# Optimization experiments

Hardware: AMD Instinct MI355X
Metric: run time of the kernel (lower is better)

Reference implementation:

```python
import jax, jax.numpy as jnp
import numpy as np

N_NODES = 100000
N_EDGES = 1600000
C = 64       # in_channels == filters
K = 3        # Chebyshev order
EPS = 1e-5   # InstanceNorm eps


def setup_inputs() -> dict:
    key = jax.random.key(0)
    ks = jax.random.split(key, 8)
    x = jax.random.normal(ks[0], (N_NODES, C), dtype=jnp.float32)
    edge_index = jax.random.randint(ks[1], (2, N_EDGES), 0, N_NODES, dtype=jnp.int64)
    scale = 1.0 / np.sqrt(C)
    W1 = jax.random.normal(ks[2], (K, C, C), dtype=jnp.float32) * scale
    b1 = jnp.zeros((C,), dtype=jnp.float32)
    W2 = jax.random.normal(ks[3], (K, C, C), dtype=jnp.float32) * scale
    b2 = jnp.zeros((C,), dtype=jnp.float32)
    return {"x": x, "edge_index": edge_index, "W1": W1, "b1": b1, "W2": W2, "b2": b2}


def _cheb_conv(x, src, dst, w_edge, W, b, n):
    # PyG ChebConv, norm='sym', lambda_max=2: L_hat = -D^{-1/2} A D^{-1/2}
    def prop(h):  # h: [N, C] -> L_hat @ h via gather -> weight -> scatter-add
        return jax.ops.segment_sum(w_edge[:, None] * h[src], dst, num_segments=n)
    Tx0 = x
    Tx1 = prop(x)
    Tx2 = 2.0 * prop(Tx1) - Tx0
    return Tx0 @ W[0] + Tx1 @ W[1] + Tx2 @ W[2] + b


def _instance_norm(h):
    # PyG InstanceNorm (single graph, affine=False): normalize over nodes per channel
    m = h.mean(axis=0, keepdims=True)
    v = h.var(axis=0, keepdims=True)
    return (h - m) * jax.lax.rsqrt(v + EPS)


def reference(x, edge_index, W1, b1, W2, b2):
    n = x.shape[0]
    src, dst = edge_index[0], edge_index[1]
    ones = jnp.ones((src.shape[0],), dtype=x.dtype)
    deg = jax.ops.segment_sum(ones, dst, num_segments=n)
    safe = jnp.where(deg > 0, deg, 1.0)
    dinv = jnp.where(deg > 0, jax.lax.rsqrt(safe), 0.0)
    w_edge = -dinv[src] * dinv[dst]  # scaled-Laplacian edge weights
    h = _instance_norm(jax.nn.relu(_cheb_conv(x, src, dst, w_edge, W1, b1, n)))
    h = _instance_norm(jax.nn.relu(_cheb_conv(h, src, dst, w_edge, W2, b2, n)))
    return h
```

## Files before the change

kernel.cpp:

```cpp
#include <hip/hip_runtime.h>
#include <hip/hip_fp16.h>

#define NCH 64
#define EPS 1e-5f
#define SBANKS 32
#define BSHIFT 8
#define NHIST 256
#define BINCAP 6400
#define PADRES 2048
#define RSHIFT 14
#define SRCMASK 0x1FFFFu
#define QW_SCALE 32767.0f
#define QW_INV (1.0f/32767.0f)

typedef _Float16 f16x8 __attribute__((ext_vector_type(8)));
typedef float f32x4 __attribute__((ext_vector_type(4)));

__global__ __launch_bounds__(256) void k_front(const float* __restrict__ x, __half* __restrict__ xh,
                                               int castTotal, int castB,
                                               const float* __restrict__ W1, _Float16* __restrict__ Wb1,
                                               const float* __restrict__ W2, _Float16* __restrict__ Wb2,
                                               const int* __restrict__ dst, int* __restrict__ cnt,
                                               int E, int per, int nbuck) {
    int bid = blockIdx.x;
    if (bid < castB) {
        int i = (bid * 256 + threadIdx.x) * 4;
        if (i < castTotal) {
            float4 f = *(const float4*)(x + i);
            __half2* o = (__half2*)(xh + i);
            o[0] = __floats2half2_rn(f.x, f.y);
            o[1] = __floats2half2_rn(f.z, f.w);
        }
        return;
    }
    if (bid < castB + 96) {
        int wb = bid - castB;
        const float* W = (wb < 48) ? W1 : W2;
        _Float16* Wb = (wb < 48) ? Wb1 : Wb2;
        int idx = (wb % 48) * 256 + threadIdx.x;
        int j = idx & 7;
        int lane = (idx >> 3) & 63;
        int tk = idx >> 9;
        int tile = tk / 6, kk = tk % 6;
        int k = kk * 32 + (lane >> 4) * 8 + j;
        int n = tile * 16 + (lane & 15);
        Wb[idx] = (_Float16)W[k * 64 + n];
        return;
    }
    __shared__ int lh[512];
    int hb = bid - castB - 96;
    for (int t = threadIdx.x; t < nbuck; t += 256) lh[t] = 0;
    __syncthreads();
    int lo = hb * per, hi = min(E, lo + per);
    for (int e = lo + threadIdx.x; e < hi; e += 256)
        atomicAdd(&lh[dst[e] >> BSHIFT], 1);
    __syncthreads();
    for (int t = threadIdx.x; t < nbuck; t += 256)
        if (lh[t]) atomicAdd(&cnt[t], lh[t]);
}

__global__ void k_bscan(const int* __restrict__ cnt, int* __restrict__ gbase,
                        int* __restrict__ gcur, int nbuck, int E) {
    __shared__ int s[512];
    int t = threadIdx.x;
    int v = (t < nbuck) ? cnt[t] : 0;
    s[t] = v;
    __syncthreads();
    for (int off = 1; off < 512; off <<= 1) {
        int add = (t >= off) ? s[t - off] : 0;
        __syncthreads();
        s[t] += add;
        __syncthreads();
    }
    if (t < nbuck) { int ex = s[t] - v; gbase[t] = ex; gcur[t] = ex; }
    if (t == 0) gbase[nbuck] = E;
}

__global__ __launch_bounds__(256) void k_bin(const int* __restrict__ src,
                                             const int* __restrict__ dst,
                                             int* __restrict__ gcur,
                                             int2* __restrict__ binned, int E, int per, int nbuck) {
    __shared__ int lh[512];
    __shared__ int lsc[512];
    __shared__ int lbase[512];
    __shared__ int lcur[512];
    __shared__ int2 sedge[BINCAP];
    int t = threadIdx.x;
    for (int i = t; i < 512; i += 256) lh[i] = 0;
    __syncthreads();
    int lo = blockIdx.x * per, hi = min(E, lo + per);
    for (int e = lo + t; e < hi; e += 256)
        atomicAdd(&lh[dst[e] >> BSHIFT], 1);
    __syncthreads();
    int v0 = lh[t], v1 = lh[t + 256];
    lsc[t] = v0; lsc[t + 256] = v1;
    __syncthreads();
    for (int off = 1; off < 512; off <<= 1) {
        int a0 = (t >= off) ? lsc[t - off] : 0;
        int a1 = (t + 256 >= off) ? lsc[t + 256 - off] : 0;
        __syncthreads();
        lsc[t] += a0; lsc[t + 256] += a1;
        __syncthreads();
    }
    lsc[t] -= v0; lsc[t + 256] -= v1;
    if (t < nbuck && v0) lbase[t] = atomicAdd(&gcur[t], v0);
    if (t + 256 < nbuck && v1) lbase[t + 256] = atomicAdd(&gcur[t + 256], v1);
    lcur[t] = lsc[t]; lcur[t + 256] = lsc[t + 256];
    __syncthreads();
    for (int e = lo + t; e < hi; e += 256) {
        int d = dst[e];
        int b = d >> BSHIFT;
        int pos = atomicAdd(&lcur[b], 1);
        sedge[pos] = make_int2(src[e], d);
    }
    __syncthreads();
    int cntE = hi - lo;
    for (int i = t; i < cntE; i += 256) {
        int2 sd = sedge[i];
        int b = sd.y >> BSHIFT;
        binned[lbase[b] + (i - lsc[b])] = sd;
    }
}

__global__ __launch_bounds__(256) void k_bucket(const int2* __restrict__ binned,
                                                const int* __restrict__ gbase,
                                                float* __restrict__ dinv,
                                                int2* __restrict__ rowinfo,
                                                unsigned int* __restrict__ csr, int N, int nbuck) {
    __shared__ int hist8[256 * 8];
    __shared__ int cur8[256 * 8];
    __shared__ int ldeg[256];
    __shared__ int ltmp[256];
    int b = blockIdx.x;
    int t = threadIdx.x;
    int nodeLo = b << BSHIFT;
    int nHere = min(256, N - nodeLo);
    int e0 = gbase[b], e1 = gbase[b + 1];
    int pb = (gbase[b] + b * PADRES + 7) & ~7;
    for (int i = t; i < 256 * 8; i += 256) hist8[i] = 0;
    __syncthreads();
    for (int e = e0 + t; e < e1; e += 256) {
        int2 sd = binned[e];
        atomicAdd(&hist8[((sd.y - nodeLo) << 3) + (sd.x >> RSHIFT)], 1);
    }
    __syncthreads();
    int c[8], deg = 0;
#pragma unroll
    for (int r = 0; r < 8; r++) { c[r] = hist8[(t << 3) + r]; deg += c[r]; }
    int pdeg = (deg + 7) & ~7;
    ldeg[t] = deg;
    if (t < nHere) dinv[nodeLo + t] = (deg > 0) ? rsqrtf((float)deg) : 0.0f;
    ltmp[t] = pdeg;
    __syncthreads();
    for (int off = 1; off < 256; off <<= 1) {
        int add = (t >= off) ? ltmp[t - off] : 0;
        __syncthreads();
        ltmp[t] += add;
        __syncthreads();
    }
    int lstart = ltmp[t] - pdeg;
    if (t < nHere) rowinfo[nodeLo + t] = make_int2(pb + lstart, pdeg);
    int run = lstart;
#pragma unroll
    for (int r = 0; r < 8; r++) { cur8[(t << 3) + r] = run; run += c[r]; }
    __syncthreads();
    for (int e = e0 + t; e < e1; e += 256) {
        int2 sd = binned[e];
        int dl = sd.y - nodeLo;
        int pos = atomicAdd(&cur8[(dl << 3) + (sd.x >> RSHIFT)], 1);
        unsigned int dd = (unsigned int)min(ldeg[dl], 32767);
        csr[pb + pos] = (unsigned int)sd.x | (dd << 17);
    }
    __syncthreads();
    if (t < nHere) {
        int d = ldeg[t];
        int pd = (d + 7) & ~7;
        if (pd > d) {
            unsigned int fill = (d > 0) ? (csr[pb + lstart] & SRCMASK) : 0u;
            for (int i = d; i < pd; i++) csr[pb + lstart + i] = fill;
        }
    }
}

__global__ void k_weights(unsigned int* __restrict__ csr, const float* __restrict__ dinv, int PE) {
    int e = blockIdx.x * blockDim.x + threadIdx.x;
    if (e < PE) {
        unsigned int v = csr[e];
        unsigned int d = v >> 17;
        if (d == 0) return;
        unsigned int s = v & SRCMASK;
        float aw = dinv[s] * rsqrtf((float)d);
        unsigned int qw = (unsigned int)(aw * QW_SCALE + 0.5f);
        csr[e] = s | (qw << 17);
    }
}


#define GATH(A0,A1,A2,A3,A4,A5,A6,A7, C0, C1) \
    A0 = *(const uint4*)(hb + (size_t)(C0.x & SRCMASK) * NCH); \
    A1 = *(const uint4*)(hb + (size_t)(C0.y & SRCMASK) * NCH); \
    A2 = *(const uint4*)(hb + (size_t)(C0.z & SRCMASK) * NCH); \
    A3 = *(const uint4*)(hb + (size_t)(C0.w & SRCMASK) * NCH); \
    A4 = *(const uint4*)(hb + (size_t)(C1.x & SRCMASK) * NCH); \
    A5 = *(const uint4*)(hb + (size_t)(C1.y & SRCMASK) * NCH); \
    A6 = *(const uint4*)(hb + (size_t)(C1.z & SRCMASK) * NCH); \
    A7 = *(const uint4*)(hb + (size_t)(C1.w & SRCMASK) * NCH);

#define FMA1(A, W) { \
    float2 f; \
    f = __half22float2(*(const __half2*)&A.x); acc[0] = fmaf(W, f.x, acc[0]); acc[1] = fmaf(W, f.y, acc[1]); \
    f = __half22float2(*(const __half2*)&A.y); acc[2] = fmaf(W, f.x, acc[2]); acc[3] = fmaf(W, f.y, acc[3]); \
    f = __half22float2(*(const __half2*)&A.z); acc[4] = fmaf(W, f.x, acc[4]); acc[5] = fmaf(W, f.y, acc[5]); \
    f = __half22float2(*(const __half2*)&A.w); acc[6] = fmaf(W, f.x, acc[6]); acc[7] = fmaf(W, f.y, acc[7]); }

#define FMA8(A0,A1,A2,A3,A4,A5,A6,A7, C0, C1) { \
    float w0 = -(float)(C0.x >> 17) * QW_INV; \
    float w1 = -(float)(C0.y >> 17) * QW_INV; \
    float w2 = -(float)(C0.z >> 17) * QW_INV; \
    float w3 = -(float)(C0.w >> 17) * QW_INV; \
    float w4 = -(float)(C1.x >> 17) * QW_INV; \
    float w5 = -(float)(C1.y >> 17) * QW_INV; \
    float w6 = -(float)(C1.z >> 17) * QW_INV; \
    float w7 = -(float)(C1.w >> 17) * QW_INV; \
    sw += ((w0 + w1) + (w2 + w3)) + ((w4 + w5) + (w6 + w7)); \
    FMA1(A0, w0) FMA1(A1, w1) FMA1(A2, w2) FMA1(A3, w3) \
    FMA1(A4, w4) FMA1(A5, w5) FMA1(A6, w6) FMA1(A7, w7) }

__global__ __launch_bounds__(256) void k_prop(const __half* __restrict__ h,
                                              const int2* __restrict__ rowinfo,
                                              const unsigned int* __restrict__ csr,
                                              const __half* __restrict__ tx0,
                                              __half* __restrict__ y, int N,
                                              const float* __restrict__ gstats,
                                              const float* __restrict__ tstats) {
    int lane = threadIdx.x & 63;
    int wv = (blockIdx.x * 256 + threadIdx.x) >> 6;
    int g = lane >> 3, li = lane & 7;
    int node = wv * 8 + g;
    int e = 0, eN = 0;
    if (node < N) {
        int2 info = rowinfo[node];
        e = info.x;
        eN = info.x + info.y;
    }
    float acc[8] = {0.f, 0.f, 0.f, 0.f, 0.f, 0.f, 0.f, 0.f};
    float sw = 0.0f;
    const __half* hb = h + li * 8;
    uint4 c0, c1, d0, d1;
    uint4 a0, a1, a2, a3, a4, a5, a6, a7;
    uint4 b0, b1, b2, b3, b4, b5, b6, b7;
    if (e < eN) {
        c0 = *(const uint4*)(csr + e);
        c1 = *(const uint4*)(csr + e + 4);
        int en = (e + 8 < eN) ? e + 8 : e;
        d0 = *(const uint4*)(csr + en);
        d1 = *(const uint4*)(csr + en + 4);
        GATH(a0, a1, a2, a3, a4, a5, a6, a7, c0, c1);
    }
    while (e + 8 < eN) {
        GATH(b0, b1, b2, b3, b4, b5, b6, b7, d0, d1);
        bool hasT = (e + 16 < eN);
        int enT = hasT ? e + 16 : e;
        uint4 t0 = *(const uint4*)(csr + enT);
        uint4 t1 = *(const uint4*)(csr + enT + 4);
        FMA8(a0, a1, a2, a3, a4, a5, a6, a7, c0, c1);
        if (hasT) { GATH(a0, a1, a2, a3, a4, a5, a6, a7, t0, t1); }
        int enD = (e + 24 < eN) ? e + 24 : e;
        uint4 u0 = *(const uint4*)(csr + enD);
        uint4 u1 = *(const uint4*)(csr + enD + 4);
        FMA8(b0, b1, b2, b3, b4, b5, b6, b7, d0, d1);
        c0 = t0; c1 = t1; d0 = u0; d1 = u1;
        e += 16;
    }
    if (e < eN) { FMA8(a0, a1, a2, a3, a4, a5, a6, a7, c0, c1); }
    if (node >= N) return;
    if (gstats != nullptr) {
        float4 m0 = *(const float4*)(gstats + li * 8);
        float4 m1 = *(const float4*)(gstats + li * 8 + 4);
        float4 r0 = *(const float4*)(gstats + 64 + li * 8);
        float4 r1 = *(const float4*)(gstats + 64 + li * 8 + 4);
        acc[0] = r0.x * (acc[0] - m0.x * sw);
        acc[1] = r0.y * (acc[1] - m0.y * sw);
        acc[2] = r0.z * (acc[2] - m0.z * sw);
        acc[3] = r0.w * (acc[3] - m0.w * sw);
        acc[4] = r1.x * (acc[4] - m1.x * sw);
        acc[5] = r1.y * (acc[5] - m1.y * sw);
        acc[6] = r1.z * (acc[6] - m1.z * sw);
        acc[7] = r1.w * (acc[7] - m1.w * sw);
    }
    if (tx0 != nullptr) {
        uint4 tq = *(const uint4*)(tx0 + (size_t)node * NCH + li * 8);
        float tv[8];
        float2 f;
        f = __half22float2(*(__half2*)&tq.x); tv[0] = f.x; tv[1] = f.y;
        f = __half22float2(*(__half2*)&tq.y); tv[2] = f.x; tv[3] = f.y;
        f = __half22float2(*(__half2*)&tq.z); tv[4] = f.x; tv[5] = f.y;
        f = __half22float2(*(__half2*)&tq.w); tv[6] = f.x; tv[7] = f.y;
        if (tstats != nullptr) {
            float4 m0 = *(const float4*)(tstats + li * 8);
            float4 m1 = *(const float4*)(tstats + li * 8 + 4);
            float4 r0 = *(const float4*)(tstats + 64 + li * 8);
            float4 r1 = *(const float4*)(tstats + 64 + li * 8 + 4);
            tv[0] = (tv[0] - m0.x) * r0.x; tv[1] = (tv[1] - m0.y) * r0.y;
            tv[2] = (tv[2] - m0.z) * r0.z; tv[3] = (tv[3] - m0.w) * r0.w;
            tv[4] = (tv[4] - m1.x) * r1.x; tv[5] = (tv[5] - m1.y) * r1.y;
            tv[6] = (tv[6] - m1.z) * r1.z; tv[7] = (tv[7] - m1.w) * r1.w;
        }
#pragma unroll
        for (int j = 0; j < 8; j++) acc[j] = 2.0f * acc[j] - tv[j];
    }
    uint4 o;
    __half2 hh;
    hh = __floats2half2_rn(acc[0], acc[1]); o.x = *(unsigned int*)&hh;
    hh = __floats2half2_rn(acc[2], acc[3]); o.y = *(unsigned int*)&hh;
    hh = __floats2half2_rn(acc[4], acc[5]); o.z = *(unsigned int*)&hh;
    hh = __floats2half2_rn(acc[6], acc[7]); o.w = *(unsigned int*)&hh;
    *(uint4*)(y + (size_t)node * NCH + li * 8) = o;
}

template <typename TOUT>
__global__ __launch_bounds__(256) void k_dmm(const __half* __restrict__ tx0,
                                             const __half* __restrict__ tx1,
                                             const __half* __restrict__ tx2,
                                             const _Float16* __restrict__ Wb,
                                             const float* __restrict__ b,
                                             TOUT* __restrict__ out,
                                             float* __restrict__ statsP, int N,
                                             const float* __restrict__ tstats) {
    __shared__ float sred[64];
    __shared__ float sq[64];
    int t = threadIdx.x;
    int w = t >> 6;
    int lane = t & 63;
    if (t < 64) { sred[t] = 0.f; sq[t] = 0.f; }
    __syncthreads();

    int nb16 = blockIdx.x * 64 + w * 16;
    int m = lane & 15, q = lane >> 4;
    int row = nb16 + m;
    int rowC = (row < N) ? row : 0;
    const __half* base0 = tx0 + (size_t)rowC * NCH;
    const __half* base1 = tx1 + (size_t)rowC * NCH;
    const __half* base2 = tx2 + (size_t)rowC * NCH;

    f32x4 acc[4];
#pragma unroll
    for (int tile = 0; tile < 4; tile++) acc[tile] = (f32x4){0.f, 0.f, 0.f, 0.f};

#pragma unroll
    for (int kk = 0; kk < 6; kk++) {
        const __half* ap = (kk < 2 ? base0 : (kk < 4 ? base1 : base2)) + (kk & 1) * 32 + q * 8;
        f16x8 a = *(const f16x8*)ap;
        if (kk < 2 && tstats != nullptr) {
            int cbase = (kk & 1) * 32 + q * 8;
#pragma unroll
            for (int j = 0; j < 8; j++) {
                float v = (float)a[j];
                a[j] = (_Float16)((v - tstats[cbase + j]) * tstats[64 + cbase + j]);
            }
        }
#pragma unroll
        for (int tile = 0; tile < 4; tile++) {
            f16x8 bf = *(const f16x8*)(Wb + ((size_t)(tile * 6 + kk) * 64 + lane) * 8);
            acc[tile] = __builtin_amdgcn_mfma_f32_16x16x32_f16(a, bf, acc[tile], 0, 0, 0);
        }
    }

#pragma unroll
    for (int tile = 0; tile < 4; tile++) {
        int ch = tile * 16 + m;
        float bb = b[ch];
        float s = 0.f, qq = 0.f;
#pragma unroll
        for (int r = 0; r < 4; r++) {
            int node = nb16 + q * 4 + r;
            float v = fmaxf(acc[tile][r] + bb, 0.f);
            if (node < N) {
                out[(size_t)node * NCH + ch] = (TOUT)v;
                s += v;
                qq = fmaf(v, v, qq);
            }
        }
        s += __shfl_xor(s, 16, 64);  s += __shfl_xor(s, 32, 64);
        qq += __shfl_xor(qq, 16, 64); qq += __shfl_xor(qq, 32, 64);
        if (q == 0) { atomicAdd(&sred[ch], s); atomicAdd(&sq[ch], qq); }
    }
    __syncthreads();
    if (t < 64) {
        int bank = blockIdx.x & (SBANKS - 1);
        atomicAdd(&statsP[bank * 128 + t], sred[t]);
        atomicAdd(&statsP[bank * 128 + 64 + t], sq[t]);
    }
}

__global__ void k_final(float* __restrict__ statsP, float invN) {
    int c = threadIdx.x;
    float S = 0.f, Q = 0.f;
    for (int k = 0; k < SBANKS; k++) {
        S += statsP[k * 128 + c];
        Q += statsP[k * 128 + 64 + c];
    }
    float m = S * invN;
    float var = Q * invN - m * m;
    statsP[SBANKS * 128 + c] = m;
    statsP[SBANKS * 128 + 64 + c] = rsqrtf(var + EPS);
}

__global__ void k_norm_hf(const __half* __restrict__ a, float* __restrict__ o,
                          const float* __restrict__ statsP, int total) {
    int i = blockIdx.x * blockDim.x + threadIdx.x;
    if (i >= total) return;
    int lane = i & 63;
    o[i] = (__half2float(a[i]) - statsP[SBANKS * 128 + lane]) * statsP[SBANKS * 128 + 64 + lane];
}

extern "C" void kernel_launch(void* const* d_in, const int* in_sizes, int n_in,
                              void* d_out, int out_size, void* d_ws, size_t ws_size,
                              hipStream_t stream) {
    const float* x  = (const float*)d_in[0];
    const int*   ei = (const int*)d_in[1];
    const float* W1 = (const float*)d_in[2];
    const float* b1 = (const float*)d_in[3];
    const float* W2 = (const float*)d_in[4];
    const float* b2 = (const float*)d_in[5];
    float* out = (float*)d_out;

    const int N = in_sizes[0] / NCH;
    const int E = in_sizes[1] / 2;
    const int* src = ei;
    const int* dst = ei + E;
    const int nbuck = (N + 255) >> BSHIFT;
    const int PE = E + nbuck * PADRES + 8;

    char* p = (char*)d_ws;
    auto alloc = [&](size_t bytes) {
        void* r = (void*)p;
        p += ((bytes + 255) / 256) * 256;
        return r;
    };
    float*  dinv     = (float*)alloc((size_t)131072 * 4);
    int2*   rowinfo  = (int2*)alloc((size_t)N * 8);
    unsigned int* csr = (unsigned int*)alloc((size_t)PE * 4);
    __half* xh       = (__half*)alloc((size_t)N * NCH * 2);
    __half* Tx1      = (__half*)alloc((size_t)N * NCH * 2);
    __half* Tx2      = (__half*)alloc((size_t)N * NCH * 2);
    __half* A        = (__half*)alloc((size_t)N * NCH * 2);
    __half* A2       = (__half*)alloc((size_t)N * NCH * 2);
    _Float16* Wb1    = (_Float16*)alloc(12288 * 2);
    _Float16* Wb2    = (_Float16*)alloc(12288 * 2);
    int*    gbase    = (int*)alloc((size_t)(nbuck + 1) * 4);
    int*    gcur     = (int*)alloc((size_t)nbuck * 4);
    const int statsFloats = SBANKS * 128 + 128;
    int*    cnt      = (int*)alloc((size_t)nbuck * 4 + (size_t)2 * statsFloats * 4);
    float*  stats1   = (float*)(cnt + nbuck);
    float*  stats2   = stats1 + statsFloats;
    const float* nrm1 = stats1 + SBANKS * 128;

    int2* binned = (int2*)Tx1;

    hipMemsetAsync(cnt, 0, (size_t)nbuck * 4 + (size_t)2 * statsFloats * 4, stream);

    const int TB = 256;
    int nbin = (E + BINCAP - 1) / BINCAP;
    if (nbin < 256) nbin = 256;
    const int perBin = (E + nbin - 1) / nbin;
    const int perH = (E + NHIST - 1) / NHIST;
    const int castTotal = N * NCH;
    const int castB = (castTotal / 4 + TB - 1) / TB;
    k_front<<<castB + 96 + NHIST, TB, 0, stream>>>(x, xh, castTotal, castB,
                                                   W1, Wb1, W2, Wb2,
                                                   dst, cnt, E, perH, nbuck);
    k_bscan<<<1, 512, 0, stream>>>(cnt, gbase, gcur, nbuck, E);
    k_bin<<<nbin, TB, 0, stream>>>(src, dst, gcur, binned, E, perBin, nbuck);
    k_bucket<<<nbuck, TB, 0, stream>>>(binned, gbase, dinv, rowinfo, csr, N, nbuck);
    k_weights<<<(PE + TB - 1) / TB, TB, 0, stream>>>(csr, dinv, PE);

    const int propWaves = (N + 7) / 8;
    const int propBlocks = (propWaves + 3) / 4;
    const int dmmBlocks = (N + 63) / 64;
    const int normBlocks = (N * NCH + TB - 1) / TB;
    const float invN = 1.0f / (float)N;

    k_prop<<<propBlocks, TB, 0, stream>>>(xh, rowinfo, csr, nullptr, Tx1, N, nullptr, nullptr);
    k_prop<<<propBlocks, TB, 0, stream>>>(Tx1, rowinfo, csr, xh, Tx2, N, nullptr, nullptr);
    k_dmm<__half><<<dmmBlocks, TB, 0, stream>>>(xh, Tx1, Tx2, Wb1, b1, A, stats1, N, nullptr);
    k_final<<<1, 64, 0, stream>>>(stats1, invN);

    k_prop<<<propBlocks, TB, 0, stream>>>(A, rowinfo, csr, nullptr, Tx1, N, nrm1, nullptr);
    k_prop<<<propBlocks, TB, 0, stream>>>(Tx1, rowinfo, csr, A, Tx2, N, nullptr, nrm1);
    k_dmm<__half><<<dmmBlocks, TB, 0, stream>>>(A, Tx1, Tx2, Wb2, b2, A2, stats2, N, nrm1);
    k_final<<<1, 64, 0, stream>>>(stats2, invN);
    k_norm_hf<<<normBlocks, TB, 0, stream>>>(A2, out, stats2, N * NCH);
}
```

Measured before the change: 341.7 us.

## Simplify prop gather loop, vectorize final norm, halve bin capacity

Result: faster. 328.8 us (-3.8%).

```diff
diff --git a/kernel.cpp b/kernel.cpp
--- a/kernel.cpp
+++ b/kernel.cpp
@@ -6,7 +6,8 @@
 #define SBANKS 32
 #define BSHIFT 8
 #define NHIST 256
-#define BINCAP 6400
+#define BINCAP 3200
+#define NBINMIN 512
 #define PADRES 2048
 #define RSHIFT 14
 #define SRCMASK 0x1FFFFu
@@ -237,42 +238,22 @@
     int wv = (blockIdx.x * 256 + threadIdx.x) >> 6;
     int g = lane >> 3, li = lane & 7;
     int node = wv * 8 + g;
-    int e = 0, eN = 0;
+    int e = 0, e1 = 0;
     if (node < N) {
         int2 info = rowinfo[node];
         e = info.x;
-        eN = info.x + info.y;
+        e1 = info.x + info.y;
     }
     float acc[8] = {0.f, 0.f, 0.f, 0.f, 0.f, 0.f, 0.f, 0.f};
     float sw = 0.0f;
     const __half* hb = h + li * 8;
-    uint4 c0, c1, d0, d1;
-    uint4 a0, a1, a2, a3, a4, a5, a6, a7;
-    uint4 b0, b1, b2, b3, b4, b5, b6, b7;
-    if (e < eN) {
-        c0 = *(const uint4*)(csr + e);
-        c1 = *(const uint4*)(csr + e + 4);
-        int en = (e + 8 < eN) ? e + 8 : e;
-        d0 = *(const uint4*)(csr + en);
-        d1 = *(const uint4*)(csr + en + 4);
+    for (; e < e1; e += 8) {
+        uint4 c0 = *(const uint4*)(csr + e);
+        uint4 c1 = *(const uint4*)(csr + e + 4);
+        uint4 a0, a1, a2, a3, a4, a5, a6, a7;
         GATH(a0, a1, a2, a3, a4, a5, a6, a7, c0, c1);
-    }
-    while (e + 8 < eN) {
-        GATH(b0, b1, b2, b3, b4, b5, b6, b7, d0, d1);
-        bool hasT = (e + 16 < eN);
-        int enT = hasT ? e + 16 : e;
-        uint4 t0 = *(const uint4*)(csr + enT);
-        uint4 t1 = *(const uint4*)(csr + enT + 4);
         FMA8(a0, a1, a2, a3, a4, a5, a6, a7, c0, c1);
-        if (hasT) { GATH(a0, a1, a2, a3, a4, a5, a6, a7, t0, t1); }
-        int enD = (e + 24 < eN) ? e + 24 : e;
-        uint4 u0 = *(const uint4*)(csr + enD);
-        uint4 u1 = *(const uint4*)(csr + enD + 4);
-        FMA8(b0, b1, b2, b3, b4, b5, b6, b7, d0, d1);
-        c0 = t0; c1 = t1; d0 = u0; d1 = u1;
-        e += 16;
-    }
-    if (e < eN) { FMA8(a0, a1, a2, a3, a4, a5, a6, a7, c0, c1); }
+    }
     if (node >= N) return;
     if (gstats != nullptr) {
         float4 m0 = *(const float4*)(gstats + li * 8);
@@ -407,11 +388,24 @@
 }
 
 __global__ void k_norm_hf(const __half* __restrict__ a, float* __restrict__ o,
-                          const float* __restrict__ statsP, int total) {
+                          const float* __restrict__ statsP, int total8) {
     int i = blockIdx.x * blockDim.x + threadIdx.x;
-    if (i >= total) return;
-    int lane = i & 63;
-    o[i] = (__half2float(a[i]) - statsP[SBANKS * 128 + lane]) * statsP[SBANKS * 128 + 64 + lane];
+    if (i >= total8) return;
+    int c0 = (i & 7) * 8;
+    const float* mp = statsP + SBANKS * 128;
+    float4 m0 = *(const float4*)(mp + c0);
+    float4 m1 = *(const float4*)(mp + c0 + 4);
+    float4 r0 = *(const float4*)(mp + 64 + c0);
+    float4 r1 = *(const float4*)(mp + 64 + c0 + 4);
+    uint4 q = *(const uint4*)(a + (size_t)i * 8);
+    float2 f;
+    float4 o0, o1;
+    f = __half22float2(*(__half2*)&q.x); o0.x = (f.x - m0.x) * r0.x; o0.y = (f.y - m0.y) * r0.y;
+    f = __half22float2(*(__half2*)&q.y); o0.z = (f.x - m0.z) * r0.z; o0.w = (f.y - m0.w) * r0.w;
+    f = __half22float2(*(__half2*)&q.z); o1.x = (f.x - m1.x) * r1.x; o1.y = (f.y - m1.y) * r1.y;
+    f = __half22float2(*(__half2*)&q.w); o1.z = (f.x - m1.z) * r1.z; o1.w = (f.y - m1.w) * r1.w;
+    *(float4*)(o + (size_t)i * 8) = o0;
+    *(float4*)(o + (size_t)i * 8 + 4) = o1;
 }
 
 extern "C" void kernel_launch(void* const* d_in, const int* in_sizes, int n_in,
@@ -462,7 +456,7 @@
 
     const int TB = 256;
     int nbin = (E + BINCAP - 1) / BINCAP;
-    if (nbin < 256) nbin = 256;
+    if (nbin < NBINMIN) nbin = NBINMIN;
     const int perBin = (E + nbin - 1) / nbin;
     const int perH = (E + NHIST - 1) / NHIST;
     const int castTotal = N * NCH;
@@ -478,7 +472,8 @@
     const int propWaves = (N + 7) / 8;
     const int propBlocks = (propWaves + 3) / 4;
     const int dmmBlocks = (N + 63) / 64;
-    const int normBlocks = (N * NCH + TB - 1) / TB;
+    const int total8 = (N * NCH) / 8;
+    const int normBlocks = (total8 + TB - 1) / TB;
     const float invN = 1.0f / (float)N;
 
     k_prop<<<propBlocks, TB, 0, stream>>>(xh, rowinfo, csr, nullptr, Tx1, N, nullptr, nullptr);
@@ -490,5 +485,5 @@
     k_prop<<<propBlocks, TB, 0, stream>>>(Tx1, rowinfo, csr, A, Tx2, N, nullptr, nrm1);
     k_dmm<__half><<<dmmBlocks, TB, 0, stream>>>(A, Tx1, Tx2, Wb2, b2, A2, stats2, N, nrm1);
     k_final<<<1, 64, 0, stream>>>(stats2, invN);
-    k_norm_hf<<<normBlocks, TB, 0, stream>>>(A2, out, stats2, N * NCH);
-}
+    k_norm_hf<<<normBlocks, TB, 0, stream>>>(A2, out, stats2, total8);
+}
```
